# Kernel optimization log

Hardware: AMD Instinct MI355X
Metric: run time of the kernel (lower is better)

The kernel has to match this reference:

```python
import jax, jax.numpy as jnp
import numpy as np

B, HW, D, CL, K, V, NL, H = 16, 4096, 512, 768, 512, 512, 32, 8
EPS = 1e-5

def conv1d(x, w, b):
    # 1x1 Conv1d: x (B, Cin, L), w (Cout, Cin), b (Cout,)
    return jnp.einsum('oi,bil->bol', w, x) + b[:, None]

def inorm(x):
    # InstanceNorm1d (affine=False, biased var) over the length dim per channel
    m = jnp.mean(x, axis=-1, keepdims=True)
    v = jnp.var(x, axis=-1, keepdims=True)
    return (x - m) / jnp.sqrt(v + EPS)

def _forward(x, l, l_mask, w_vis, b_vis, w_langp, b_langp, w_q, b_q, w_k, b_k,
             w_v, b_v, w_lv, b_lv, w_W, b_W, w_langW, b_langW,
             w_mm, b_mm, w_langmm, b_langmm):
    xt = x.transpose(0, 2, 1)                       # (B, D, HW)
    mask = l_mask.transpose(0, 2, 1)                # (B, 1, NL)
    vis = jax.nn.gelu(conv1d(xt, w_vis, b_vis), approximate=False)      # (B, D, HW)
    lang = jax.nn.gelu(conv1d(l, w_langp, b_langp), approximate=False)  # (B, CL, NL)

    q = inorm(conv1d(xt, w_q, b_q)).transpose(0, 2, 1)   # (B, HW, K)
    k = conv1d(l, w_k, b_k) * mask                       # (B, K, NL)
    v = conv1d(l, w_v, b_v) * mask                       # (B, V, NL)
    lv = inorm(conv1d(xt, w_lv, b_lv))                   # (B, CL, HW)

    q = q.reshape(B, HW, H, K // H).transpose(0, 2, 1, 3)   # (B, H, HW, dk)
    k = k.reshape(B, H, K // H, NL)
    v = v.reshape(B, H, V // H, NL)
    lv = lv.reshape(B, H, CL // H, HW)

    # note: scale uses FULL key_channels (as in the torch code), mask bias added once
    sim = jnp.einsum('bhqd,bhdn->bhqn', q, k) * (K ** -0.5)
    sim = sim + (10000.0 * mask[:, :, None, :] - 10000.0)    # (B, H, HW, NL)

    att = jax.nn.softmax(sim, axis=-1)                         # image -> lang
    latt = jax.nn.softmax(sim.transpose(0, 1, 3, 2), axis=-1)  # lang -> image

    lang_out = jnp.einsum('bhnq,bhcq->bhcn', latt, lv).reshape(B, CL, NL) * mask
    lang_out = inorm(conv1d(lang_out, w_langW, b_langW))       # (B, CL, NL)

    out = jnp.einsum('bhqn,bhdn->bqhd', att, v).reshape(B, HW, V)
    vis_out = inorm(conv1d(out.transpose(0, 2, 1), w_W, b_W))  # (B, V, HW)

    mm = jax.nn.gelu(conv1d(vis * vis_out, w_mm, b_mm), approximate=False)
    lang_mm = jax.nn.gelu(conv1d(lang * lang_out, w_langmm, b_langmm), approximate=False)
    return mm.transpose(0, 2, 1), lang_mm.transpose(0, 2, 1)   # (B,HW,V), (B,NL,CL)

def setup_inputs():
    key = jax.random.key(0)
    ks = jax.random.split(key, 24)
    inp = {}
    inp['x'] = jax.random.normal(ks[0], (B, HW, D), jnp.float32)
    inp['l'] = jax.random.normal(ks[1], (B, CL, NL), jnp.float32)
    lengths = jax.random.randint(ks[2], (B, 1), 5, NL + 1)
    inp['l_mask'] = (jnp.arange(NL)[None, :] < lengths).astype(jnp.float32)[:, :, None]
    specs = [('vis', D, D), ('langp', CL, CL), ('q', K, D), ('k', K, CL),
             ('v', V, CL), ('lv', CL, D), ('W', V, V), ('langW', CL, CL),
             ('mm', V, V), ('langmm', CL, CL)]
    for i, (n, o, ci) in enumerate(specs):
        inp['w_' + n] = jax.random.normal(ks[3 + 2 * i], (o, ci), jnp.float32) / float(np.sqrt(ci))
        inp['b_' + n] = jax.random.normal(ks[4 + 2 * i], (o,), jnp.float32) * 0.01
    return inp

def reference(x, l, l_mask, w_vis, b_vis, w_langp, b_langp, w_q, b_q, w_k, b_k,
              w_v, b_v, w_lv, b_lv, w_W, b_W, w_langW, b_langW,
              w_mm, b_mm, w_langmm, b_langmm):
    return _forward(x, l, l_mask, w_vis, b_vis, w_langp, b_langp, w_q, b_q, w_k, b_k,
                    w_v, b_v, w_lv, b_lv, w_W, b_W, w_langW, b_langW,
                    w_mm, b_mm, w_langmm, b_langmm)
```

## Files before the change

### kernel.cpp

```cpp
#include <hip/hip_runtime.h>
#include <cstdint>
#include <cstddef>


typedef __bf16 bf16x8 __attribute__((ext_vector_type(8)));
typedef float f32x4 __attribute__((ext_vector_type(4)));
typedef unsigned short ushort8 __attribute__((ext_vector_type(8)));
typedef unsigned short us4 __attribute__((ext_vector_type(4)));

__device__ __forceinline__ float bf2f(unsigned short u) {
  union { unsigned int i; float f; } c; c.i = ((unsigned int)u) << 16; return c.f;
}
__device__ __forceinline__ unsigned short f2bf(float f) {
  union { float f; unsigned int i; } c; c.f = f;
  unsigned int r = c.i + 0x7FFFu + ((c.i >> 16) & 1u);
  return (unsigned short)(r >> 16);
}
__device__ __forceinline__ float gelu_f(float x) {
  return 0.5f * x * (1.f + erff(x * 0.70710678118654752f));
}
__device__ __forceinline__ void gload16(const void* g, void* l) {
  __builtin_amdgcn_global_load_lds(
      (__attribute__((address_space(1))) unsigned int*)g,
      (__attribute__((address_space(3))) unsigned int*)l, 16, 0, 0);
}
__device__ __forceinline__ int xcd_swizzle(int orig, int nwg) {
  int qd = nwg >> 3, r = nwg & 7;
  int xcd = orig & 7, idx = orig >> 3;
  return (xcd < r ? xcd * (qd + 1) : r * (qd + 1) + (xcd - r) * qd) + idx;
}

constexpr size_t OFF_SRQ  = 0;
constexpr size_t OFF_SRLV = OFF_SRQ  + (size_t)16*512*2*4;
constexpr size_t OFF_SRW  = OFF_SRLV + (size_t)16*768*2*4;
constexpr size_t OFF_LACC = OFF_SRW  + (size_t)16*512*2*4;
constexpr size_t SZ_ZERO  = OFF_LACC + (size_t)16*768*32*4;
constexpr size_t OFF_STQ  = SZ_ZERO;
constexpr size_t OFF_STLV = OFF_STQ  + (size_t)16*512*2*4;
constexpr size_t OFF_STW  = OFF_STLV + (size_t)16*768*2*4;
constexpr size_t OFF_KBUF = OFF_STW  + (size_t)16*512*2*4;
constexpr size_t OFF_VBUF = OFF_KBUF + (size_t)16*512*32*4;
constexpr size_t OFF_LANG = OFF_VBUF + (size_t)16*512*32*4;
constexpr size_t OFF_LMX  = OFF_LANG + (size_t)16*768*32*4;
constexpr size_t OFF_LSM  = OFF_LMX  + (size_t)128*32*4;
constexpr size_t OFF_LNORM= OFF_LSM  + (size_t)128*32*4;
constexpr size_t OFF_P2   = OFF_LNORM+ (size_t)16*768*32*4;
constexpr size_t OFF_PMX  = OFF_P2   + (size_t)16*768*32*4;
constexpr size_t OFF_PSM  = OFF_PMX  + (size_t)32*128*32*4;
constexpr size_t OFF_WB   = OFF_PSM  + (size_t)32*128*32*4;
constexpr size_t OFF_Q    = OFF_WB   + (size_t)1441792*2;
constexpr size_t OFF_LV   = OFF_Q    + (size_t)65536*512*2;
constexpr size_t OFF_SIMB = OFF_LV   + (size_t)65536*768*2;

__global__ __launch_bounds__(256) void cvt_bf16(const float* __restrict__ src,
                                                unsigned short* __restrict__ dst, int n8)
{
  int i = blockIdx.x * 256 + threadIdx.x;
  if (i >= n8) return;
  const f32x4* s = (const f32x4*)(src + (size_t)i * 8);
  f32x4 a = s[0], b = s[1];
  ushort8 o;
#pragma unroll
  for (int j = 0; j < 4; ++j) { o[j] = f2bf(a[j]); o[j + 4] = f2bf(b[j]); }
  *(ushort8*)(dst + (size_t)i * 8) = o;
}

template<bool GELU, bool STATS, bool OUTF32>
__global__ __launch_bounds__(256) void gemm_bt(
    const unsigned short* __restrict__ A, const unsigned short* __restrict__ Wb,
    const float* __restrict__ bias, void* __restrict__ Yout,
    float* __restrict__ statsraw, int N, int Kd, int nbn)
{
  __shared__ __align__(16) unsigned short As[128 * 64];
  __shared__ __align__(16) unsigned short Bs[128 * 64];
  const int t = threadIdx.x;
  const int wave = t >> 6, lane = t & 63;
  const int ln = lane & 15, quad = lane >> 4;
  const int wgid = xcd_swizzle(blockIdx.x, gridDim.x);
  const int mt = wgid / nbn, nt = wgid - mt * nbn;
  const int m0 = mt * 128, n0 = nt * 128;
  const int wm = (wave >> 1) * 64, wn = (wave & 1) * 64;
  const f32x4 fzero = {0.f, 0.f, 0.f, 0.f};
  f32x4 acc[4][4];
#pragma unroll
  for (int i = 0; i < 4; ++i)
#pragma unroll
    for (int j = 0; j < 4; ++j) acc[i][j] = fzero;
  const int lrow = lane >> 3;
  const int lch  = lane & 7;

  for (int k0 = 0; k0 < Kd; k0 += 64) {
#pragma unroll
    for (int it = 0; it < 4; ++it) {
      int g = wave * 4 + it;
      int row = g * 8 + lrow;
      gload16(A  + (size_t)(m0 + row) * Kd + k0 + lch * 8, &As[g * 512]);
      gload16(Wb + (size_t)(n0 + row) * Kd + k0 + lch * 8, &Bs[g * 512]);
    }
    __syncthreads();
#pragma unroll
    for (int kk = 0; kk < 64; kk += 32) {
      int c = (kk >> 3) + quad;
      bf16x8 af[4], bfr[4];
#pragma unroll
      for (int i = 0; i < 4; ++i)
        af[i] = *(const bf16x8*)&As[(wm + i * 16 + ln) * 64 + c * 8];
#pragma unroll
      for (int j = 0; j < 4; ++j)
        bfr[j] = *(const bf16x8*)&Bs[(wn + j * 16 + ln) * 64 + c * 8];
#pragma unroll
      for (int i = 0; i < 4; ++i)
#pragma unroll
        for (int j = 0; j < 4; ++j)
          acc[i][j] = __builtin_amdgcn_mfma_f32_16x16x32_bf16(af[i], bfr[j], acc[i][j], 0, 0, 0);
    }
    __syncthreads();
  }
  float bb[4];
#pragma unroll
  for (int j = 0; j < 4; ++j) bb[j] = bias[n0 + wn + j * 16 + ln];
#pragma unroll
  for (int i = 0; i < 4; ++i)
#pragma unroll
    for (int j = 0; j < 4; ++j)
#pragma unroll
      for (int r = 0; r < 4; ++r) {
        float v = acc[i][j][r] + bb[j];
        if (GELU) v = gelu_f(v);
        acc[i][j][r] = v;
        size_t row = (size_t)(m0 + wm + i * 16 + quad * 4 + r);
        size_t idx = row * N + (n0 + wn + j * 16 + ln);
        if (OUTF32) ((float*)Yout)[idx] = v;
        else ((unsigned short*)Yout)[idx] = f2bf(v);
      }
  if (STATS) {
    float* cs = (float*)As;
    cs[t] = 0.f;
    __syncthreads();
#pragma unroll
    for (int j = 0; j < 4; ++j) {
      float s = 0.f, s2 = 0.f;
#pragma unroll
      for (int i = 0; i < 4; ++i)
#pragma unroll
        for (int r = 0; r < 4; ++r) { float v = acc[i][j][r]; s += v; s2 += v * v; }
      int cl = wn + j * 16 + ln;
      atomicAdd(&cs[cl], s);
      atomicAdd(&cs[128 + cl], s2);
    }
    __syncthreads();
    int bIdx = m0 >> 12;
    if (t < 128) atomicAdd(&statsraw[((size_t)bIdx * N + n0 + t) * 2], cs[t]);
    else atomicAdd(&statsraw[((size_t)bIdx * N + n0 + (t - 128)) * 2 + 1], cs[t]);
  }
}

__global__ __launch_bounds__(256) void gemm_fused3(
    const unsigned short* __restrict__ A, const unsigned short* __restrict__ Wcat,
    const float* __restrict__ b_vis, const float* __restrict__ b_q, const float* __restrict__ b_lv,
    unsigned short* __restrict__ visb, unsigned short* __restrict__ qout,
    unsigned short* __restrict__ lvout, float* __restrict__ srq, float* __restrict__ srlv)
{
  constexpr int NBN = 14, Kd = 512;
  __shared__ __align__(16) unsigned short As[128 * 64];
  __shared__ __align__(16) unsigned short Bs[128 * 64];
  const int t = threadIdx.x;
  const int wave = t >> 6, lane = t & 63;
  const int ln = lane & 15, quad = lane >> 4;
  const int wgid = xcd_swizzle(blockIdx.x, gridDim.x);
  const int mt = wgid / NBN, nt = wgid - mt * NBN;
  const int m0 = mt * 128, n0 = nt * 128;
  const int wm = (wave >> 1) * 64, wn = (wave & 1) * 64;
  const f32x4 fzero = {0.f, 0.f, 0.f, 0.f};
  f32x4 acc[4][4];
#pragma unroll
  for (int i = 0; i < 4; ++i)
#pragma unroll
    for (int j = 0; j < 4; ++j) acc[i][j] = fzero;
  const int lrow = lane >> 3;
  const int lch  = lane & 7;

  for (int k0 = 0; k0 < Kd; k0 += 64) {
#pragma unroll
    for (int it = 0; it < 4; ++it) {
      int g = wave * 4 + it;
      int row = g * 8 + lrow;
      gload16(A    + (size_t)(m0 + row) * Kd + k0 + lch * 8, &As[g * 512]);
      gload16(Wcat + (size_t)(n0 + row) * Kd + k0 + lch * 8, &Bs[g * 512]);
    }
    __syncthreads();
#pragma unroll
    for (int kk = 0; kk < 64; kk += 32) {
      int c = (kk >> 3) + quad;
      bf16x8 af[4], bfr[4];
#pragma unroll
      for (int i = 0; i < 4; ++i)
        af[i] = *(const bf16x8*)&As[(wm + i * 16 + ln) * 64 + c * 8];
#pragma unroll
      for (int j = 0; j < 4; ++j)
        bfr[j] = *(const bf16x8*)&Bs[(wn + j * 16 + ln) * 64 + c * 8];
#pragma unroll
      for (int i = 0; i < 4; ++i)
#pragma unroll
        for (int j = 0; j < 4; ++j)
          acc[i][j] = __builtin_amdgcn_mfma_f32_16x16x32_bf16(af[i], bfr[j], acc[i][j], 0, 0, 0);
    }
    __syncthreads();
  }
  int seg = (nt < 4) ? 0 : (nt < 8 ? 1 : 2);
  const float* bias = (seg == 0) ? b_vis : (seg == 1 ? b_q : b_lv);
  unsigned short* Y = (seg == 0) ? visb : (seg == 1 ? qout : lvout);
  float* statsraw   = (seg == 1) ? srq : srlv;
  const int nbase   = n0 - ((seg == 0) ? 0 : (seg == 1 ? 512 : 1024));
  const int Nseg    = (seg == 2) ? 768 : 512;

  float bb[4];
#pragma unroll
  for (int j = 0; j < 4; ++j) bb[j] = bias[nbase + wn + j * 16 + ln];
#pragma unroll
  for (int i = 0; i < 4; ++i)
#pragma unroll
    for (int j = 0; j < 4; ++j)
#pragma unroll
      for (int r = 0; r < 4; ++r) {
        float v = acc[i][j][r] + bb[j];
        if (seg == 0) v = gelu_f(v);
        acc[i][j][r] = v;
        size_t row = (size_t)(m0 + wm + i * 16 + quad * 4 + r);
        Y[row * Nseg + (nbase + wn + j * 16 + ln)] = f2bf(v);
      }
  if (seg != 0) {
    float* cs = (float*)As;
    cs[t] = 0.f;
    __syncthreads();
#pragma unroll
    for (int j = 0; j < 4; ++j) {
      float s = 0.f, s2 = 0.f;
#pragma unroll
      for (int i = 0; i < 4; ++i)
#pragma unroll
        for (int r = 0; r < 4; ++r) { float v = acc[i][j][r]; s += v; s2 += v * v; }
      int cl = wn + j * 16 + ln;
      atomicAdd(&cs[cl], s);
      atomicAdd(&cs[128 + cl], s2);
    }
    __syncthreads();
    int bIdx = m0 >> 12;
    if (t < 128) atomicAdd(&statsraw[((size_t)bIdx * Nseg + nbase + t) * 2], cs[t]);
    else atomicAdd(&statsraw[((size_t)bIdx * Nseg + nbase + (t - 128)) * 2 + 1], cs[t]);
  }
}

__global__ void finalize_stats(const float* __restrict__ raw, float* __restrict__ st,
                               int n, float invc) {
  int i = blockIdx.x * 256 + threadIdx.x;
  if (i >= n) return;
  float s = raw[2 * i], s2 = raw[2 * i + 1];
  float m = s * invc;
  float v = fmaxf(s2 * invc - m * m, 0.f);
  st[2 * i] = m;
  st[2 * i + 1] = rsqrtf(v + 1e-5f);
}

template<int EPI>
__global__ __launch_bounds__(256) void sconv(
    const float* __restrict__ l, const float* __restrict__ w,
    const float* __restrict__ bias, const float* __restrict__ lmask,
    float* __restrict__ out, int O, int Cin)
{
  int b = blockIdx.x, og = blockIdx.y;
  int ol = threadIdx.x >> 5, n = threadIdx.x & 31;
  int o = og * 8 + ol;
  const float* lb = l + (size_t)b * Cin * 32 + n;
  const float* wr = w + (size_t)o * Cin;
  float s = 0.f;
#pragma unroll 4
  for (int i = 0; i < Cin; ++i) s += wr[i] * lb[(size_t)i * 32];
  s += bias[o];
  if (EPI == 0) s *= lmask[b * 32 + n];
  else s = gelu_f(s);
  out[((size_t)b * O + o) * 32 + n] = s;
}

__global__ __launch_bounds__(256) void simattv_kernel(
    const unsigned short* __restrict__ qraw, const float* __restrict__ stq,
    const float* __restrict__ kbuf, const float* __restrict__ vbuf,
    const float* __restrict__ lmask,
    unsigned short* __restrict__ simb, unsigned short* __restrict__ outb,
    float* __restrict__ pmx, float* __restrict__ psm)
{
  __shared__ __align__(16) unsigned short kThi[32][72];
  __shared__ __align__(16) unsigned short kTlo[32][72];
  __shared__ __align__(16) unsigned short vshi[64][40];
  __shared__ __align__(16) unsigned short vslo[64][40];
  __shared__ __align__(16) unsigned short pq[4][32][40];
  __shared__ float sm[64], srs[64], cb[32];
  __shared__ float wmax[4][32], wsum[4][32];

  const int qc = blockIdx.x, q0 = qc * 128, h = blockIdx.y, b = blockIdx.z;
  const int bh = b * 8 + h;
  const int t = threadIdx.x;
  const int wv = t >> 6, lane = t & 63, ln = lane & 15, quad = lane >> 4;
  const float scale = 0.04419417382415922f;

  if (t < 64) {
    sm[t]  = stq[(b * 512 + h * 64 + t) * 2];
    srs[t] = stq[(b * 512 + h * 64 + t) * 2 + 1] * scale;
  }
  __syncthreads();

  const float* kb = kbuf + ((size_t)b * 512 + h * 64) * 32;
  const float* vb = vbuf + ((size_t)b * 512 + h * 64) * 32;
  for (int e = t; e < 2048; e += 256) {
    int d = e >> 5, n = e & 31;
    float kv = kb[e] * srs[d];
    unsigned short khi = f2bf(kv);
    kThi[n][d] = khi;
    kTlo[n][d] = f2bf(kv - bf2f(khi));
    float vv = vb[e];
    unsigned short vhi = f2bf(vv);
    vshi[d][n] = vhi;
    vslo[d][n] = f2bf(vv - bf2f(vhi));
  }
  if (t < 32) {
    float s = 0.f;
#pragma unroll 8
    for (int d = 0; d < 64; ++d) s += sm[d] * srs[d] * kb[d * 32 + t];
    cb[t] = 10000.f * (lmask[b * 32 + t] - 1.f) - s;
  }

  const unsigned short* qbase = qraw + ((size_t)(b * 4096) + q0 + wv * 32) * 512 + h * 64;
  bf16x8 qfr[2][2];
#pragma unroll
  for (int qf = 0; qf < 2; ++qf)
#pragma unroll
    for (int kf = 0; kf < 2; ++kf)
      qfr[qf][kf] = *(const bf16x8*)(qbase + (size_t)(qf * 16 + ln) * 512 + kf * 32 + quad * 8);
  __syncthreads();

  const f32x4 fz = {0.f, 0.f, 0.f, 0.f};
  f32x4 accS[2][2] = {{fz, fz}, {fz, fz}};
#pragma unroll
  for (int kf = 0; kf < 2; ++kf) {
#pragma unroll
    for (int nf = 0; nf < 2; ++nf) {
      bf16x8 kh = *(const bf16x8*)&kThi[nf * 16 + ln][kf * 32 + quad * 8];
      bf16x8 kl = *(const bf16x8*)&kTlo[nf * 16 + ln][kf * 32 + quad * 8];
#pragma unroll
      for (int qf = 0; qf < 2; ++qf) {
        accS[qf][nf] = __builtin_amdgcn_mfma_f32_16x16x32_bf16(qfr[qf][kf], kh, accS[qf][nf], 0, 0, 0);
        accS[qf][nf] = __builtin_amdgcn_mfma_f32_16x16x32_bf16(qfr[qf][kf], kl, accS[qf][nf], 0, 0, 0);
      }
    }
  }
  float cb0 = cb[ln], cb1 = cb[16 + ln];
#pragma unroll
  for (int qf = 0; qf < 2; ++qf)
#pragma unroll
    for (int r = 0; r < 4; ++r) {
      accS[qf][0][r] += cb0;
      accS[qf][1][r] += cb1;
    }
  {
    unsigned short* sgb = simb + ((size_t)bh * 4096 + q0 + wv * 32) * 32;
#pragma unroll
    for (int qf = 0; qf < 2; ++qf)
#pragma unroll
      for (int r = 0; r < 4; ++r) {
        size_t rowo = (size_t)(qf * 16 + quad * 4 + r) * 32;
        sgb[rowo + ln]      = f2bf(accS[qf][0][r]);
        sgb[rowo + 16 + ln] = f2bf(accS[qf][1][r]);
      }
  }
#pragma unroll
  for (int nf = 0; nf < 2; ++nf) {
    float m = accS[0][nf][0];
#pragma unroll
    for (int r = 1; r < 4; ++r) m = fmaxf(m, accS[0][nf][r]);
#pragma unroll
    for (int r = 0; r < 4; ++r) m = fmaxf(m, accS[1][nf][r]);
    m = fmaxf(m, __shfl_xor(m, 16));
    m = fmaxf(m, __shfl_xor(m, 32));
    float s = 0.f;
#pragma unroll
    for (int qf = 0; qf < 2; ++qf)
#pragma unroll
      for (int r = 0; r < 4; ++r) s += __expf(accS[qf][nf][r] - m);
    s += __shfl_xor(s, 16);
    s += __shfl_xor(s, 32);
    if (quad == 0) { wmax[wv][nf * 16 + ln] = m; wsum[wv][nf * 16 + ln] = s; }
  }
#pragma unroll
  for (int qf = 0; qf < 2; ++qf) {
#pragma unroll
    for (int r = 0; r < 4; ++r) {
      float a0 = accS[qf][0][r], a1 = accS[qf][1][r];
      float m = fmaxf(a0, a1);
      m = fmaxf(m, __shfl_xor(m, 1));
      m = fmaxf(m, __shfl_xor(m, 2));
      m = fmaxf(m, __shfl_xor(m, 4));
      m = fmaxf(m, __shfl_xor(m, 8));
      float e0 = __expf(a0 - m), e1 = __expf(a1 - m);
      float s = e0 + e1;
      s += __shfl_xor(s, 1);
      s += __shfl_xor(s, 2);
      s += __shfl_xor(s, 4);
      s += __shfl_xor(s, 8);
      float inv = 1.f / s;
      int row = qf * 16 + quad * 4 + r;
      pq[wv][row][ln]      = f2bf(e0 * inv);
      pq[wv][row][16 + ln] = f2bf(e1 * inv);
    }
  }
  __syncthreads();
  bf16x8 vfh[4], vfl[4];
#pragma unroll
  for (int mf = 0; mf < 4; ++mf) {
    vfh[mf] = *(const bf16x8*)&vshi[mf * 16 + ln][quad * 8];
    vfl[mf] = *(const bf16x8*)&vslo[mf * 16 + ln][quad * 8];
  }
#pragma unroll
  for (int nf = 0; nf < 2; ++nf) {
    bf16x8 pb = *(const bf16x8*)&pq[wv][nf * 16 + ln][quad * 8];
    f32x4 accO[4] = {fz, fz, fz, fz};
#pragma unroll
    for (int mf = 0; mf < 4; ++mf) {
      accO[mf] = __builtin_amdgcn_mfma_f32_16x16x32_bf16(vfh[mf], pb, accO[mf], 0, 0, 0);
      accO[mf] = __builtin_amdgcn_mfma_f32_16x16x32_bf16(vfl[mf], pb, accO[mf], 0, 0, 0);
    }
    unsigned short* op = outb + ((size_t)(b * 4096) + q0 + wv * 32 + nf * 16 + ln) * 512 + h * 64;
#pragma unroll
    for (int mf = 0; mf < 4; ++mf) {
      us4 o;
#pragma unroll
      for (int r = 0; r < 4; ++r) o[r] = f2bf(accO[mf][r]);
      *(us4*)(op + mf * 16 + quad * 4) = o;
    }
  }
  __syncthreads();
  if (t < 32) {
    float M = wmax[0][t], S = wsum[0][t];
#pragma unroll
    for (int g = 1; g < 4; ++g) {
      float m2 = wmax[g][t], s2 = wsum[g][t];
      if (m2 > M) { S = S * __expf(M - m2) + s2; M = m2; }
      else S += s2 * __expf(m2 - M);
    }
    pmx[((size_t)qc * 128 + bh) * 32 + t] = M;
    psm[((size_t)qc * 128 + bh) * 32 + t] = S;
  }
}

__global__ __launch_bounds__(256) void latt_merge(const float* __restrict__ pmx,
                                                  const float* __restrict__ psm,
                                                  float* __restrict__ lmx,
                                                  float* __restrict__ lsm)
{
  int i = blockIdx.x * 256 + threadIdx.x;
  int bh = i >> 5, n = i & 31;
  float M = -1e30f, S = 0.f;
#pragma unroll 4
  for (int c = 0; c < 32; ++c) {
    float m2 = pmx[((size_t)c * 128 + bh) * 32 + n];
    float s2 = psm[((size_t)c * 128 + bh) * 32 + n];
    if (m2 > M) { S = S * __expf(M - m2) + s2; M = m2; }
    else S += s2 * __expf(m2 - M);
  }
  lmx[bh * 32 + n] = M;
  lsm[bh * 32 + n] = S;
}

__global__ __launch_bounds__(256) void langout_acc_kernel(
    const unsigned short* __restrict__ simb, const float* __restrict__ lmx,
    const float* __restrict__ lsm, const unsigned short* __restrict__ lvraw,
    const float* __restrict__ stlv, float* __restrict__ lacc)
{
  __shared__ __align__(16) float pt[64][32];
  __shared__ __align__(16) float lvt[64][96];
  __shared__ float cm[96], cr[96], lm[32], li[32];
  int bh = blockIdx.x, b = bh >> 3, h = bh & 7;
  int qs0 = blockIdx.y * 512;
  int t = threadIdx.x;
  if (t < 96) { cm[t] = stlv[(b * 768 + h * 96 + t) * 2]; cr[t] = stlv[(b * 768 + h * 96 + t) * 2 + 1]; }
  else if (t >= 128 && t < 160) {
    int n = t - 128;
    lm[n] = lmx[bh * 32 + n];
    li[n] = 1.f / lsm[bh * 32 + n];
  }
  __syncthreads();
  int n = t & 31, cg = t >> 5;
  float acc[12];
#pragma unroll
  for (int r = 0; r < 12; ++r) acc[r] = 0.f;
  for (int c0 = 0; c0 < 512; c0 += 64) {
    if (c0) __syncthreads();
#pragma unroll
    for (int i = 0; i < 8; ++i) {
      int e = t + 256 * i;
      int ql = e >> 5, nn = e & 31;
      float x = bf2f(simb[((size_t)bh * 4096 + qs0 + c0 + ql) * 32 + nn]);
      pt[ql][nn] = __expf(x - lm[nn]) * li[nn];
    }
#pragma unroll
    for (int i = 0; i < 24; ++i) {
      int e = t + 256 * i;
      int ql = e / 96, cc = e % 96;
      float v = bf2f(lvraw[((size_t)(b * 4096) + qs0 + c0 + ql) * 768 + h * 96 + cc]);
      lvt[ql][cc] = (v - cm[cc]) * cr[cc];
    }
    __syncthreads();
    for (int q = 0; q < 64; ++q) {
      float pv = pt[q][n];
      const f32x4* lp = (const f32x4*)&lvt[q][cg * 12];
      f32x4 a0 = lp[0], a1 = lp[1], a2 = lp[2];
      acc[0] += pv * a0[0]; acc[1] += pv * a0[1]; acc[2]  += pv * a0[2]; acc[3]  += pv * a0[3];
      acc[4] += pv * a1[0]; acc[5] += pv * a1[1]; acc[6]  += pv * a1[2]; acc[7]  += pv * a1[3];
      acc[8] += pv * a2[0]; acc[9] += pv * a2[1]; acc[10] += pv * a2[2]; acc[11] += pv * a2[3];
    }
  }
#pragma unroll
  for (int r = 0; r < 12; ++r)
    atomicAdd(&lacc[((size_t)b * 768 + h * 96 + cg * 12 + r) * 32 + n], acc[r]);
}

__global__ __launch_bounds__(256) void prod_kernel(
    const unsigned short* __restrict__ visb, const unsigned short* __restrict__ wraw,
    const float* __restrict__ stw, unsigned short* __restrict__ P)
{
  size_t idx = ((size_t)blockIdx.x * 256 + threadIdx.x) * 8;
  int b = (int)(idx >> 21);
  int c = (int)(idx & 511);
  ushort8 vv = *(const ushort8*)&visb[idx];
  ushort8 wv = *(const ushort8*)&wraw[idx];
  ushort8 pv;
#pragma unroll
  for (int i = 0; i < 8; ++i) {
    float mean = stw[(b * 512 + c + i) * 2], rs = stw[(b * 512 + c + i) * 2 + 1];
    pv[i] = f2bf(bf2f(vv[i]) * ((bf2f(wv[i]) - mean) * rs));
  }
  *(ushort8*)&P[idx] = pv;
}

__global__ __launch_bounds__(256) void langW_kernel(
    const float* __restrict__ lacc, const float* __restrict__ w,
    const float* __restrict__ bias, const float* __restrict__ lmask,
    float* __restrict__ lnorm)
{
  int b = blockIdx.x, og = blockIdx.y;
  int ol = threadIdx.x >> 5, n = threadIdx.x & 31;
  int o = og * 8 + ol;
  const float* ab = lacc + (size_t)b * 768 * 32 + n;
  const float* wr = w + (size_t)o * 768;
  float s = 0.f;
#pragma unroll 4
  for (int i = 0; i < 768; ++i) s += wr[i] * ab[(size_t)i * 32];
  float y = s * lmask[b * 32 + n] + bias[o];
  float m = y;
#pragma unroll
  for (int off = 16; off >= 1; off >>= 1) m += __shfl_xor(m, off);
  m *= (1.f / 32.f);
  float d = y - m;
  float vv = d * d;
#pragma unroll
  for (int off = 16; off >= 1; off >>= 1) vv += __shfl_xor(vv, off);
  vv *= (1.f / 32.f);
  lnorm[((size_t)b * 768 + o) * 32 + n] = d * rsqrtf(vv + 1e-5f);
}

__global__ __launch_bounds__(256) void p2_kernel(const float* __restrict__ a,
                                                 const float* __restrict__ b,
                                                 float* __restrict__ o, int n) {
  int i = blockIdx.x * 256 + threadIdx.x;
  if (i < n) o[i] = a[i] * b[i];
}

__global__ __launch_bounds__(256) void langmm_kernel(
    const float* __restrict__ p2, const float* __restrict__ w,
    const float* __restrict__ bias, float* __restrict__ out1)
{
  int b = blockIdx.x, og = blockIdx.y;
  int ol = threadIdx.x >> 5, n = threadIdx.x & 31;
  int o = og * 8 + ol;
  const float* pb = p2 + (size_t)b * 768 * 32 + n;
  const float* wr = w + (size_t)o * 768;
  float s = 0.f;
#pragma unroll 4
  for (int i = 0; i < 768; ++i) s += wr[i] * pb[(size_t)i * 32];
  s = gelu_f(s + bias[o]);
  __shared__ float tile[8][32];
  tile[ol][n] = s;
  __syncthreads();
  int nn = threadIdx.x >> 3, cl = threadIdx.x & 7;
  out1[((size_t)b * 32 + nn) * 768 + og * 8 + cl] = tile[cl][nn];
}

extern "C" void kernel_launch(void* const* d_in, const int* in_sizes, int n_in,
                              void* d_out, int out_size, void* d_ws, size_t ws_size,
                              hipStream_t stream)
{
  (void)in_sizes; (void)n_in; (void)out_size; (void)ws_size;
  const float* x       = (const float*)d_in[0];
  const float* l       = (const float*)d_in[1];
  const float* lmask   = (const float*)d_in[2];
  const float* w_vis   = (const float*)d_in[3];
  const float* b_vis   = (const float*)d_in[4];
  const float* w_langp = (const float*)d_in[5];
  const float* b_langp = (const float*)d_in[6];
  const float* w_q     = (const float*)d_in[7];
  const float* b_q     = (const float*)d_in[8];
  const float* w_k     = (const float*)d_in[9];
  const float* b_k     = (const float*)d_in[10];
  const float* w_v     = (const float*)d_in[11];
  const float* b_v     = (const float*)d_in[12];
  const float* w_lv    = (const float*)d_in[13];
  const float* b_lv    = (const float*)d_in[14];
  const float* w_W     = (const float*)d_in[15];
  const float* b_W     = (const float*)d_in[16];
  const float* w_langW = (const float*)d_in[17];
  const float* b_langW = (const float*)d_in[18];
  const float* w_mm    = (const float*)d_in[19];
  const float* b_mm    = (const float*)d_in[20];
  const float* w_langmm= (const float*)d_in[21];
  const float* b_langmm= (const float*)d_in[22];

  char* ws = (char*)d_ws;
  float* srq  = (float*)(ws + OFF_SRQ);
  float* srlv = (float*)(ws + OFF_SRLV);
  float* srw  = (float*)(ws + OFF_SRW);
  float* lacc = (float*)(ws + OFF_LACC);
  float* stq  = (float*)(ws + OFF_STQ);
  float* stlv = (float*)(ws + OFF_STLV);
  float* stw  = (float*)(ws + OFF_STW);
  float* kbuf = (float*)(ws + OFF_KBUF);
  float* vbuf = (float*)(ws + OFF_VBUF);
  float* lang = (float*)(ws + OFF_LANG);
  float* lmx  = (float*)(ws + OFF_LMX);
  float* lsm  = (float*)(ws + OFF_LSM);
  float* lnorm= (float*)(ws + OFF_LNORM);
  float* p2   = (float*)(ws + OFF_P2);
  float* pmx  = (float*)(ws + OFF_PMX);
  float* psm  = (float*)(ws + OFF_PSM);
  unsigned short* wb    = (unsigned short*)(ws + OFF_WB);
  unsigned short* wbvis = wb;
  unsigned short* wbq   = wb + 262144;
  unsigned short* wblv  = wb + 524288;
  unsigned short* wbW   = wb + 917504;
  unsigned short* wbmm  = wb + 1179648;
  unsigned short* qraw  = (unsigned short*)(ws + OFF_Q);
  unsigned short* lvraw = (unsigned short*)(ws + OFF_LV);
  unsigned short* wraw  = (unsigned short*)(ws + OFF_LV);
  unsigned short* simb  = (unsigned short*)(ws + OFF_SIMB);
  float* out0 = (float*)d_out;
  float* out1 = out0 + (size_t)16 * 4096 * 512;
  unsigned short* visb = (unsigned short*)d_out;
  unsigned short* xb   = (unsigned short*)d_out + 33554432;

  hipMemsetAsync(ws, 0, SZ_ZERO, stream);

  cvt_bf16<<<16384, 256, 0, stream>>>(x, xb, 4194304);
  cvt_bf16<<<128, 256, 0, stream>>>(w_vis, wbvis, 32768);
  cvt_bf16<<<128, 256, 0, stream>>>(w_q,   wbq,   32768);
  cvt_bf16<<<192, 256, 0, stream>>>(w_lv,  wblv,  49152);
  cvt_bf16<<<128, 256, 0, stream>>>(w_W,   wbW,   32768);
  cvt_bf16<<<128, 256, 0, stream>>>(w_mm,  wbmm,  32768);

  sconv<1><<<dim3(16, 96), 256, 0, stream>>>(l, w_langp, b_langp, lmask, lang, 768, 768);
  sconv<0><<<dim3(16, 64), 256, 0, stream>>>(l, w_k, b_k, lmask, kbuf, 512, 768);
  sconv<0><<<dim3(16, 64), 256, 0, stream>>>(l, w_v, b_v, lmask, vbuf, 512, 768);

  gemm_fused3<<<512 * 14, 256, 0, stream>>>(xb, wb, b_vis, b_q, b_lv,
                                            visb, qraw, lvraw, srq, srlv);
  finalize_stats<<<32, 256, 0, stream>>>(srq,  stq,  16 * 512, 1.f / 4096.f);
  finalize_stats<<<48, 256, 0, stream>>>(srlv, stlv, 16 * 768, 1.f / 4096.f);

  simattv_kernel<<<dim3(32, 8, 16), 256, 0, stream>>>(qraw, stq, kbuf, vbuf, lmask, simb, qraw, pmx, psm);
  latt_merge<<<16, 256, 0, stream>>>(pmx, psm, lmx, lsm);
  langout_acc_kernel<<<dim3(128, 8), 256, 0, stream>>>(simb, lmx, lsm, lvraw, stlv, lacc);

  gemm_bt<false, true,  false><<<512 * 4, 256, 0, stream>>>(qraw, wbW, b_W, wraw, srw, 512, 512, 4);
  finalize_stats<<<32, 256, 0, stream>>>(srw, stw, 16 * 512, 1.f / 4096.f);
  prod_kernel<<<16384, 256, 0, stream>>>(visb, wraw, stw, qraw);
  gemm_bt<true,  false, true ><<<512 * 4, 256, 0, stream>>>(qraw, wbmm, b_mm, out0, nullptr, 512, 512, 4);

  langW_kernel<<<dim3(16, 96), 256, 0, stream>>>(lacc, w_langW, b_langW, lmask, lnorm);
  p2_kernel<<<1536, 256, 0, stream>>>(lang, lnorm, p2, 16 * 768 * 32);
  langmm_kernel<<<dim3(16, 96), 256, 0, stream>>>(p2, w_langmm, b_langmm, out1);
}
```

Baseline: 1.279 ms.

## Fuse prep, stats finalize, softmax merge and elementwise kernels to cut launches

The memset, six bf16 conversions and three small language convs are merged into one prep kernel that also zeroes the accumulation workspace. The finalize_stats, latt_merge and p2 kernels are removed, and their math is inlined into the consumer kernels (simattv, langout_acc, prod, langW). The GEMM stats epilogue now reduces across quads with shuffles before issuing LDS atomics, so fewer atomics are issued. This cuts roughly ten launches and some global round-trips. In exchange, prod_kernel recomputes rsqrt per element, and the prep kernel has divergent block roles.

```diff
diff --git a/kernel.cpp b/kernel.cpp
--- a/kernel.cpp
+++ b/kernel.cpp
@@ -35,16 +35,10 @@
 constexpr size_t OFF_SRW  = OFF_SRLV + (size_t)16*768*2*4;
 constexpr size_t OFF_LACC = OFF_SRW  + (size_t)16*512*2*4;
 constexpr size_t SZ_ZERO  = OFF_LACC + (size_t)16*768*32*4;
-constexpr size_t OFF_STQ  = SZ_ZERO;
-constexpr size_t OFF_STLV = OFF_STQ  + (size_t)16*512*2*4;
-constexpr size_t OFF_STW  = OFF_STLV + (size_t)16*768*2*4;
-constexpr size_t OFF_KBUF = OFF_STW  + (size_t)16*512*2*4;
+constexpr size_t OFF_KBUF = SZ_ZERO;
 constexpr size_t OFF_VBUF = OFF_KBUF + (size_t)16*512*32*4;
 constexpr size_t OFF_LANG = OFF_VBUF + (size_t)16*512*32*4;
-constexpr size_t OFF_LMX  = OFF_LANG + (size_t)16*768*32*4;
-constexpr size_t OFF_LSM  = OFF_LMX  + (size_t)128*32*4;
-constexpr size_t OFF_LNORM= OFF_LSM  + (size_t)128*32*4;
-constexpr size_t OFF_P2   = OFF_LNORM+ (size_t)16*768*32*4;
+constexpr size_t OFF_P2   = OFF_LANG + (size_t)16*768*32*4;
 constexpr size_t OFF_PMX  = OFF_P2   + (size_t)16*768*32*4;
 constexpr size_t OFF_PSM  = OFF_PMX  + (size_t)32*128*32*4;
 constexpr size_t OFF_WB   = OFF_PSM  + (size_t)32*128*32*4;
@@ -52,17 +46,75 @@
 constexpr size_t OFF_LV   = OFF_Q    + (size_t)65536*512*2;
 constexpr size_t OFF_SIMB = OFF_LV   + (size_t)65536*768*2;
 
-__global__ __launch_bounds__(256) void cvt_bf16(const float* __restrict__ src,
-                                                unsigned short* __restrict__ dst, int n8)
-{
-  int i = blockIdx.x * 256 + threadIdx.x;
-  if (i >= n8) return;
-  const f32x4* s = (const f32x4*)(src + (size_t)i * 8);
-  f32x4 a = s[0], b = s[1];
-  ushort8 o;
-#pragma unroll
-  for (int j = 0; j < 4; ++j) { o[j] = f2bf(a[j]); o[j + 4] = f2bf(b[j]); }
-  *(ushort8*)(dst + (size_t)i * 8) = o;
+__global__ __launch_bounds__(256) void prep_kernel(
+    const float* __restrict__ x,
+    const float* __restrict__ w_vis, const float* __restrict__ w_q,
+    const float* __restrict__ w_lv, const float* __restrict__ w_W,
+    const float* __restrict__ w_mm,
+    unsigned short* __restrict__ xb, unsigned short* __restrict__ wb,
+    const float* __restrict__ l,
+    const float* __restrict__ w_langp, const float* __restrict__ b_langp,
+    const float* __restrict__ w_k, const float* __restrict__ b_k,
+    const float* __restrict__ w_v, const float* __restrict__ b_v,
+    const float* __restrict__ lmask,
+    float* __restrict__ lang, float* __restrict__ kbuf, float* __restrict__ vbuf,
+    float* __restrict__ zbase)
+{
+  const int bid = blockIdx.x, t = threadIdx.x;
+  if (bid < 17088) {
+    int i = bid * 256 + t;
+    if (i >= 4374528) return;
+    const float* src;
+    unsigned short* dst;
+    if (i < 4194304) { src = x + (size_t)i * 8; dst = xb + (size_t)i * 8; }
+    else {
+      int j = i - 4194304;
+      dst = wb + (size_t)j * 8;
+      if (j < 32768)       src = w_vis + (size_t)j * 8;
+      else if (j < 65536)  src = w_q  + (size_t)(j - 32768) * 8;
+      else if (j < 114688) src = w_lv + (size_t)(j - 65536) * 8;
+      else if (j < 147456) src = w_W  + (size_t)(j - 114688) * 8;
+      else                 src = w_mm + (size_t)(j - 147456) * 8;
+    }
+    const f32x4* s = (const f32x4*)src;
+    f32x4 a = s[0], b2 = s[1];
+    ushort8 o;
+#pragma unroll
+    for (int j = 0; j < 4; ++j) { o[j] = f2bf(a[j]); o[j + 4] = f2bf(b2[j]); }
+    *(ushort8*)dst = o;
+  } else if (bid < 20672) {
+    int sb = bid - 17088;
+    int b = sb & 15, og = sb >> 4;
+    int ol = t >> 5, n = t & 31;
+    const float* lb = l + (size_t)b * 768 * 32 + n;
+    const float* wr;
+    float bv;
+    float* out;
+    bool gel;
+    if (og < 96) {
+      int o = og * 8 + ol;
+      wr = w_langp + (size_t)o * 768; bv = b_langp[o];
+      out = &lang[((size_t)b * 768 + o) * 32 + n]; gel = true;
+    } else if (og < 160) {
+      int o = (og - 96) * 8 + ol;
+      wr = w_k + (size_t)o * 768; bv = b_k[o];
+      out = &kbuf[((size_t)b * 512 + o) * 32 + n]; gel = false;
+    } else {
+      int o = (og - 160) * 8 + ol;
+      wr = w_v + (size_t)o * 768; bv = b_v[o];
+      out = &vbuf[((size_t)b * 512 + o) * 32 + n]; gel = false;
+    }
+    float s = 0.f;
+#pragma unroll 4
+    for (int i = 0; i < 768; ++i) s += wr[i] * lb[(size_t)i * 32];
+    s += bv;
+    s = gel ? gelu_f(s) : s * lmask[b * 32 + n];
+    *out = s;
+  } else {
+    size_t i = (size_t)(bid - 20672) * 256 + t;
+    const f32x4 z = {0.f, 0.f, 0.f, 0.f};
+    ((f32x4*)zbase)[i] = z;
+  }
 }
 
 template<bool GELU, bool STATS, bool OUTF32>
@@ -144,9 +196,13 @@
       for (int i = 0; i < 4; ++i)
 #pragma unroll
         for (int r = 0; r < 4; ++r) { float v = acc[i][j][r]; s += v; s2 += v * v; }
-      int cl = wn + j * 16 + ln;
-      atomicAdd(&cs[cl], s);
-      atomicAdd(&cs[128 + cl], s2);
+      s  += __shfl_xor(s, 16);  s  += __shfl_xor(s, 32);
+      s2 += __shfl_xor(s2, 16); s2 += __shfl_xor(s2, 32);
+      if (quad == 0) {
+        int cl = wn + j * 16 + ln;
+        atomicAdd(&cs[cl], s);
+        atomicAdd(&cs[128 + cl], s2);
+      }
     }
     __syncthreads();
     int bIdx = m0 >> 12;
@@ -240,9 +296,13 @@
       for (int i = 0; i < 4; ++i)
 #pragma unroll
         for (int r = 0; r < 4; ++r) { float v = acc[i][j][r]; s += v; s2 += v * v; }
-      int cl = wn + j * 16 + ln;
-      atomicAdd(&cs[cl], s);
-      atomicAdd(&cs[128 + cl], s2);
+      s  += __shfl_xor(s, 16);  s  += __shfl_xor(s, 32);
+      s2 += __shfl_xor(s2, 16); s2 += __shfl_xor(s2, 32);
+      if (quad == 0) {
+        int cl = wn + j * 16 + ln;
+        atomicAdd(&cs[cl], s);
+        atomicAdd(&cs[128 + cl], s2);
+      }
     }
     __syncthreads();
     int bIdx = m0 >> 12;
@@ -251,39 +311,8 @@
   }
 }
 
-__global__ void finalize_stats(const float* __restrict__ raw, float* __restrict__ st,
-                               int n, float invc) {
-  int i = blockIdx.x * 256 + threadIdx.x;
-  if (i >= n) return;
-  float s = raw[2 * i], s2 = raw[2 * i + 1];
-  float m = s * invc;
-  float v = fmaxf(s2 * invc - m * m, 0.f);
-  st[2 * i] = m;
-  st[2 * i + 1] = rsqrtf(v + 1e-5f);
-}
-
-template<int EPI>
-__global__ __launch_bounds__(256) void sconv(
-    const float* __restrict__ l, const float* __restrict__ w,
-    const float* __restrict__ bias, const float* __restrict__ lmask,
-    float* __restrict__ out, int O, int Cin)
-{
-  int b = blockIdx.x, og = blockIdx.y;
-  int ol = threadIdx.x >> 5, n = threadIdx.x & 31;
-  int o = og * 8 + ol;
-  const float* lb = l + (size_t)b * Cin * 32 + n;
-  const float* wr = w + (size_t)o * Cin;
-  float s = 0.f;
-#pragma unroll 4
-  for (int i = 0; i < Cin; ++i) s += wr[i] * lb[(size_t)i * 32];
-  s += bias[o];
-  if (EPI == 0) s *= lmask[b * 32 + n];
-  else s = gelu_f(s);
-  out[((size_t)b * O + o) * 32 + n] = s;
-}
-
 __global__ __launch_bounds__(256) void simattv_kernel(
-    const unsigned short* __restrict__ qraw, const float* __restrict__ stq,
+    const unsigned short* __restrict__ qraw, const float* __restrict__ srq,
     const float* __restrict__ kbuf, const float* __restrict__ vbuf,
     const float* __restrict__ lmask,
     unsigned short* __restrict__ simb, unsigned short* __restrict__ outb,
@@ -304,8 +333,12 @@
   const float scale = 0.04419417382415922f;
 
   if (t < 64) {
-    sm[t]  = stq[(b * 512 + h * 64 + t) * 2];
-    srs[t] = stq[(b * 512 + h * 64 + t) * 2 + 1] * scale;
+    float s  = srq[(b * 512 + h * 64 + t) * 2];
+    float s2 = srq[(b * 512 + h * 64 + t) * 2 + 1];
+    float mean = s * (1.f / 4096.f);
+    float var  = fmaxf(s2 * (1.f / 4096.f) - mean * mean, 0.f);
+    sm[t]  = mean;
+    srs[t] = rsqrtf(var + 1e-5f) * scale;
   }
   __syncthreads();
 
@@ -451,29 +484,10 @@
   }
 }
 
-__global__ __launch_bounds__(256) void latt_merge(const float* __restrict__ pmx,
-                                                  const float* __restrict__ psm,
-                                                  float* __restrict__ lmx,
-                                                  float* __restrict__ lsm)
-{
-  int i = blockIdx.x * 256 + threadIdx.x;
-  int bh = i >> 5, n = i & 31;
-  float M = -1e30f, S = 0.f;
-#pragma unroll 4
-  for (int c = 0; c < 32; ++c) {
-    float m2 = pmx[((size_t)c * 128 + bh) * 32 + n];
-    float s2 = psm[((size_t)c * 128 + bh) * 32 + n];
-    if (m2 > M) { S = S * __expf(M - m2) + s2; M = m2; }
-    else S += s2 * __expf(m2 - M);
-  }
-  lmx[bh * 32 + n] = M;
-  lsm[bh * 32 + n] = S;
-}
-
 __global__ __launch_bounds__(256) void langout_acc_kernel(
-    const unsigned short* __restrict__ simb, const float* __restrict__ lmx,
-    const float* __restrict__ lsm, const unsigned short* __restrict__ lvraw,
-    const float* __restrict__ stlv, float* __restrict__ lacc)
+    const unsigned short* __restrict__ simb, const float* __restrict__ pmx,
+    const float* __restrict__ psm, const unsigned short* __restrict__ lvraw,
+    const float* __restrict__ srlv, float* __restrict__ lacc)
 {
   __shared__ __align__(16) float pt[64][32];
   __shared__ __align__(16) float lvt[64][96];
@@ -481,11 +495,25 @@
   int bh = blockIdx.x, b = bh >> 3, h = bh & 7;
   int qs0 = blockIdx.y * 512;
   int t = threadIdx.x;
-  if (t < 96) { cm[t] = stlv[(b * 768 + h * 96 + t) * 2]; cr[t] = stlv[(b * 768 + h * 96 + t) * 2 + 1]; }
-  else if (t >= 128 && t < 160) {
+  if (t < 96) {
+    float s  = srlv[(b * 768 + h * 96 + t) * 2];
+    float s2 = srlv[(b * 768 + h * 96 + t) * 2 + 1];
+    float mean = s * (1.f / 4096.f);
+    float var  = fmaxf(s2 * (1.f / 4096.f) - mean * mean, 0.f);
+    cm[t] = mean;
+    cr[t] = rsqrtf(var + 1e-5f);
+  } else if (t >= 128 && t < 160) {
     int n = t - 128;
-    lm[n] = lmx[bh * 32 + n];
-    li[n] = 1.f / lsm[bh * 32 + n];
+    float M = -1e30f, S = 0.f;
+#pragma unroll 4
+    for (int c = 0; c < 32; ++c) {
+      float m2 = pmx[((size_t)c * 128 + bh) * 32 + n];
+      float s2 = psm[((size_t)c * 128 + bh) * 32 + n];
+      if (m2 > M) { S = S * __expf(M - m2) + s2; M = m2; }
+      else S += s2 * __expf(m2 - M);
+    }
+    lm[n] = M;
+    li[n] = 1.f / S;
   }
   __syncthreads();
   int n = t & 31, cg = t >> 5;
@@ -525,7 +553,7 @@
 
 __global__ __launch_bounds__(256) void prod_kernel(
     const unsigned short* __restrict__ visb, const unsigned short* __restrict__ wraw,
-    const float* __restrict__ stw, unsigned short* __restrict__ P)
+    const float* __restrict__ srw, unsigned short* __restrict__ P)
 {
   size_t idx = ((size_t)blockIdx.x * 256 + threadIdx.x) * 8;
   int b = (int)(idx >> 21);
@@ -535,7 +563,11 @@
   ushort8 pv;
 #pragma unroll
   for (int i = 0; i < 8; ++i) {
-    float mean = stw[(b * 512 + c + i) * 2], rs = stw[(b * 512 + c + i) * 2 + 1];
+    float s  = srw[(b * 512 + c + i) * 2];
+    float s2 = srw[(b * 512 + c + i) * 2 + 1];
+    float mean = s * (1.f / 4096.f);
+    float var  = fmaxf(s2 * (1.f / 4096.f) - mean * mean, 0.f);
+    float rs   = rsqrtf(var + 1e-5f);
     pv[i] = f2bf(bf2f(vv[i]) * ((bf2f(wv[i]) - mean) * rs));
   }
   *(ushort8*)&P[idx] = pv;
@@ -544,7 +576,7 @@
 __global__ __launch_bounds__(256) void langW_kernel(
     const float* __restrict__ lacc, const float* __restrict__ w,
     const float* __restrict__ bias, const float* __restrict__ lmask,
-    float* __restrict__ lnorm)
+    const float* __restrict__ lang, float* __restrict__ p2)
 {
   int b = blockIdx.x, og = blockIdx.y;
   int ol = threadIdx.x >> 5, n = threadIdx.x & 31;
@@ -564,14 +596,8 @@
 #pragma unroll
   for (int off = 16; off >= 1; off >>= 1) vv += __shfl_xor(vv, off);
   vv *= (1.f / 32.f);
-  lnorm[((size_t)b * 768 + o) * 32 + n] = d * rsqrtf(vv + 1e-5f);
-}
-
-__global__ __launch_bounds__(256) void p2_kernel(const float* __restrict__ a,
-                                                 const float* __restrict__ b,
-                                                 float* __restrict__ o, int n) {
-  int i = blockIdx.x * 256 + threadIdx.x;
-  if (i < n) o[i] = a[i] * b[i];
+  size_t idx = ((size_t)b * 768 + o) * 32 + n;
+  p2[idx] = lang[idx] * (d * rsqrtf(vv + 1e-5f));
 }
 
 __global__ __launch_bounds__(256) void langmm_kernel(
@@ -628,22 +654,13 @@
   float* srlv = (float*)(ws + OFF_SRLV);
   float* srw  = (float*)(ws + OFF_SRW);
   float* lacc = (float*)(ws + OFF_LACC);
-  float* stq  = (float*)(ws + OFF_STQ);
-  float* stlv = (float*)(ws + OFF_STLV);
-  float* stw  = (float*)(ws + OFF_STW);
   float* kbuf = (float*)(ws + OFF_KBUF);
   float* vbuf = (float*)(ws + OFF_VBUF);
   float* lang = (float*)(ws + OFF_LANG);
-  float* lmx  = (float*)(ws + OFF_LMX);
-  float* lsm  = (float*)(ws + OFF_LSM);
-  float* lnorm= (float*)(ws + OFF_LNORM);
   float* p2   = (float*)(ws + OFF_P2);
   float* pmx  = (float*)(ws + OFF_PMX);
   float* psm  = (float*)(ws + OFF_PSM);
   unsigned short* wb    = (unsigned short*)(ws + OFF_WB);
-  unsigned short* wbvis = wb;
-  unsigned short* wbq   = wb + 262144;
-  unsigned short* wblv  = wb + 524288;
   unsigned short* wbW   = wb + 917504;
   unsigned short* wbmm  = wb + 1179648;
   unsigned short* qraw  = (unsigned short*)(ws + OFF_Q);
@@ -655,34 +672,20 @@
   unsigned short* visb = (unsigned short*)d_out;
   unsigned short* xb   = (unsigned short*)d_out + 33554432;
 
-  hipMemsetAsync(ws, 0, SZ_ZERO, stream);
-
-  cvt_bf16<<<16384, 256, 0, stream>>>(x, xb, 4194304);
-  cvt_bf16<<<128, 256, 0, stream>>>(w_vis, wbvis, 32768);
-  cvt_bf16<<<128, 256, 0, stream>>>(w_q,   wbq,   32768);
-  cvt_bf16<<<192, 256, 0, stream>>>(w_lv,  wblv,  49152);
-  cvt_bf16<<<128, 256, 0, stream>>>(w_W,   wbW,   32768);
-  cvt_bf16<<<128, 256, 0, stream>>>(w_mm,  wbmm,  32768);
-
-  sconv<1><<<dim3(16, 96), 256, 0, stream>>>(l, w_langp, b_langp, lmask, lang, 768, 768);
-  sconv<0><<<dim3(16, 64), 256, 0, stream>>>(l, w_k, b_k, lmask, kbuf, 512, 768);
-  sconv<0><<<dim3(16, 64), 256, 0, stream>>>(l, w_v, b_v, lmask, vbuf, 512, 768);
+  prep_kernel<<<21112, 256, 0, stream>>>(x, w_vis, w_q, w_lv, w_W, w_mm, xb, wb,
+                                         l, w_langp, b_langp, w_k, b_k, w_v, b_v,
+                                         lmask, lang, kbuf, vbuf, (float*)ws);
 
   gemm_fused3<<<512 * 14, 256, 0, stream>>>(xb, wb, b_vis, b_q, b_lv,
                                             visb, qraw, lvraw, srq, srlv);
-  finalize_stats<<<32, 256, 0, stream>>>(srq,  stq,  16 * 512, 1.f / 4096.f);
-  finalize_stats<<<48, 256, 0, stream>>>(srlv, stlv, 16 * 768, 1.f / 4096.f);
-
-  simattv_kernel<<<dim3(32, 8, 16), 256, 0, stream>>>(qraw, stq, kbuf, vbuf, lmask, simb, qraw, pmx, psm);
-  latt_merge<<<16, 256, 0, stream>>>(pmx, psm, lmx, lsm);
-  langout_acc_kernel<<<dim3(128, 8), 256, 0, stream>>>(simb, lmx, lsm, lvraw, stlv, lacc);
+
+  simattv_kernel<<<dim3(32, 8, 16), 256, 0, stream>>>(qraw, srq, kbuf, vbuf, lmask, simb, qraw, pmx, psm);
+  langout_acc_kernel<<<dim3(128, 8), 256, 0, stream>>>(simb, pmx, psm, lvraw, srlv, lacc);
 
   gemm_bt<false, true,  false><<<512 * 4, 256, 0, stream>>>(qraw, wbW, b_W, wraw, srw, 512, 512, 4);
-  finalize_stats<<<32, 256, 0, stream>>>(srw, stw, 16 * 512, 1.f / 4096.f);
-  prod_kernel<<<16384, 256, 0, stream>>>(visb, wraw, stw, qraw);
+  prod_kernel<<<16384, 256, 0, stream>>>(visb, wraw, srw, qraw);
   gemm_bt<true,  false, true ><<<512 * 4, 256, 0, stream>>>(qraw, wbmm, b_mm, out0, nullptr, 512, 512, 4);
 
-  langW_kernel<<<dim3(16, 96), 256, 0, stream>>>(lacc, w_langW, b_langW, lmask, lnorm);
-  p2_kernel<<<1536, 256, 0, stream>>>(lang, lnorm, p2, 16 * 768 * 32);
+  langW_kernel<<<dim3(16, 96), 256, 0, stream>>>(lacc, w_langW, b_langW, lmask, lang, p2);
   langmm_kernel<<<dim3(16, 96), 256, 0, stream>>>(p2, w_langmm, b_langmm, out1);
 }
```

After: 1.319 ms. 1.03x slower.
